# Performance work log

Hardware: AMD Instinct MI355X
Metric: run time of the kernel (lower is better)

Reference implementation:

```python
import jax, jax.numpy as jnp
import numpy as np

B = 8
N_GENES = 19836
D_IN = 11
D_H = 64
DEG = 16
N = B * N_GENES
E_PER = N_GENES * DEG


def setup_inputs() -> dict:
    key = jax.random.key(0)
    ks = jax.random.split(key, 20)
    x = jax.random.normal(ks[0], (B, N_GENES, D_IN), dtype=jnp.float32)
    # edges: random within each graph, offset by graph index
    base_src = jax.random.randint(ks[1], (B, E_PER), 0, N_GENES)
    base_dst = jax.random.randint(ks[2], (B, E_PER), 0, N_GENES)
    offs = (jnp.arange(B) * N_GENES)[:, None]
    src = (base_src + offs).reshape(-1).astype(jnp.int64) if False else (base_src + offs).reshape(-1)
    dst = (base_dst + offs).reshape(-1)
    s = 0.02
    def nrm(k, shape):
        return jax.random.normal(k, shape, dtype=jnp.float32) * s
    return {
        'x': x, 'src': src, 'dst': dst,
        'enc_W': nrm(ks[3], (D_H, D_IN)), 'enc_b': jnp.zeros((D_H,), jnp.float32),
        'gene_emb': nrm(ks[4], (N_GENES, D_H)),
        'gin_W': nrm(ks[5], (D_H, D_H)),
        'bn_w': 1.0 + nrm(ks[6], (D_H,)), 'bn_b': jnp.zeros((D_H,), jnp.float32),
        'key_W': nrm(ks[7], (D_H, D_H)), 'key_b': jnp.zeros((D_H,), jnp.float32),
        'query_w': nrm(ks[8], (1, D_H)),
        'val_W': nrm(ks[9], (D_H, D_H)), 'val_b': jnp.zeros((D_H,), jnp.float32),
        'sae_enc_W': nrm(ks[10], (D_H, D_H)), 'sae_enc_b': jnp.zeros((D_H,), jnp.float32),
        'sae_dec_W': nrm(ks[11], (D_H, D_H)), 'sae_dec_b': jnp.zeros((D_H,), jnp.float32),
        'pred_W1': nrm(ks[12], (D_H, D_H)), 'pred_b1': jnp.zeros((D_H,), jnp.float32),
        'pred_W2': nrm(ks[13], (1, D_H)), 'pred_b2': jnp.zeros((1,), jnp.float32),
    }


def gelu(x):
    return jax.nn.gelu(x, approximate=False)  # nn.GELU default = exact erf


def batchnorm(h, w, b, eps=1e-5):
    # training-mode BatchNorm1d: batch statistics, biased variance
    mu = jnp.mean(h, axis=0)
    var = jnp.mean((h - mu) ** 2, axis=0)
    return (h - mu) * jax.lax.rsqrt(var + eps) * w + b


def reference(x, src, dst, enc_W, enc_b, gene_emb, gin_W, bn_w, bn_b,
              key_W, key_b, query_w, val_W, val_b,
              sae_enc_W, sae_enc_b, sae_dec_W, sae_dec_b,
              pred_W1, pred_b1, pred_W2, pred_b2):
    bsz, n_gene, d_in = x.shape
    n_nodes = bsz * n_gene
    # gene encoder: single Linear (bias) + GELU (inner batchnorm result is discarded in source)
    h = gelu(x.reshape(-1, d_in) @ enc_W.T + enc_b)          # [N, D_H]
    h = (h.reshape(bsz, n_gene, -1) + gene_emb).reshape(n_nodes, -1)
    # GIN layer (eps=0, sum aggregation): MLP(h + sum_{u->v} h_u); MLP = single Linear, no bias
    agg = jax.ops.segment_sum(h[src], dst, num_segments=n_nodes)  # irregular gather/scatter
    h = (h + agg) @ gin_W.T
    h = gelu(batchnorm(h, bn_w, bn_b))
    # attentive readout with SAE
    keys = h @ key_W.T + key_b
    w = jax.nn.sigmoid(keys @ query_w.T)                     # [N, 1]
    v = h @ val_W.T + val_b
    z = v * w
    enc = jax.nn.relu(z @ sae_enc_W.T + sae_enc_b)
    dec = enc @ sae_dec_W.T + sae_dec_b
    sae_loss = jnp.mean((dec - z) ** 2) + 1.0 * jnp.mean(jnp.abs(enc))
    gid = jnp.arange(n_nodes) // n_gene
    g_h = jax.ops.segment_sum(dec * w, gid, num_segments=bsz)  # [B, D_H]
    # predictor: Linear+GELU, Linear (inner batchnorm discarded in source)
    preds = gelu(g_h @ pred_W1.T + pred_b1) @ pred_W2.T + pred_b2
    return preds, w, sae_loss, dec
```

## Files before the change

### kernel.cpp

```cpp
#include <hip/hip_runtime.h>
#include <hip/hip_bf16.h>
#include <math.h>

#define NGENES 19836
#define BATCH 8
#define DIN 11
#define DH 64
#define NNODES (BATCH * NGENES)
#define E_PER (NGENES * 16)
#define NEDGES (NNODES * 16)
#define NDH (NNODES * DH)
#define NWAVE ((NNODES + 63) / 64)
#define NBLK_NODE ((NWAVE + 3) / 4)

#define SCAN_CHUNK 1024
#define NSBLK ((NNODES + SCAN_CHUNK - 1) / SCAN_CHUNK)

#define OUT_PREDS 0
#define OUT_W 8
#define OUT_SAE (8 + NNODES)
#define OUT_DEC (9 + NNODES)

__device__ __forceinline__ float gelu_f(float x) {
    return 0.5f * x * (1.0f + erff(x * 0.70710678118654752f));
}

__device__ __forceinline__ float bcast(float v, int lane) {
    return __int_as_float(__builtin_amdgcn_readlane(__float_as_int(v), lane));
}

__device__ __forceinline__ float wave_sum(float v) {
    #pragma unroll
    for (int o = 32; o; o >>= 1) v += __shfl_xor(v, o, 64);
    return v;
}

__global__ void k_encoder(const float* __restrict__ x, const float* __restrict__ encW,
                          const float* __restrict__ encB, const float* __restrict__ gemb,
                          __hip_bfloat16* __restrict__ h16) {
    int lane = threadIdx.x & 63;
    int g = blockIdx.x & 7;
    int wix = (blockIdx.x >> 3) * (blockDim.x >> 6) + (threadIdx.x >> 6);
    int wper = (gridDim.x >> 3) * (blockDim.x >> 6);
    float wreg[DIN];
    #pragma unroll
    for (int k = 0; k < DIN; ++k) wreg[k] = encW[lane * DIN + k];
    float bias = encB[lane];
    size_t gb = (size_t)g * NGENES;
    for (int i = wix; i < NGENES; i += wper) {
        size_t node = gb + i;
        const float* xr = x + node * DIN;
        float acc = bias;
        #pragma unroll
        for (int k = 0; k < DIN; ++k) acc = fmaf(xr[k], wreg[k], acc);
        float hv = gelu_f(acc) + gemb[(size_t)i * DH + lane];
        h16[node * DH + lane] = __float2bfloat16(hv);
    }
}

__global__ void k_hist(const int* __restrict__ dst, int* __restrict__ counts) {
    int g = blockIdx.x & 7;
    int t = (blockIdx.x >> 3) * blockDim.x + threadIdx.x;
    int nt = (gridDim.x >> 3) * blockDim.x;
    const int* dg = dst + (size_t)g * E_PER;
    for (int e = t; e < E_PER; e += nt)
        atomicAdd(&counts[dg[e]], 1);
}

__global__ void k_scan1(const int* __restrict__ counts, int* __restrict__ bsum) {
    __shared__ int red[256];
    int base = blockIdx.x * SCAN_CHUNK + threadIdx.x * 4;
    int s = 0;
    #pragma unroll
    for (int i = 0; i < 4; ++i) {
        int n = base + i;
        if (n < NNODES) s += counts[n];
    }
    red[threadIdx.x] = s;
    __syncthreads();
    for (int o = 128; o; o >>= 1) {
        if (threadIdx.x < o) red[threadIdx.x] += red[threadIdx.x + o];
        __syncthreads();
    }
    if (threadIdx.x == 0) bsum[blockIdx.x] = red[0];
}

__global__ void k_scan2(const int* __restrict__ bsum, int* __restrict__ boff) {
    __shared__ int red[256];
    int t = threadIdx.x;
    int v = (t < NSBLK) ? bsum[t] : 0;
    red[t] = v;
    __syncthreads();
    for (int o = 1; o < 256; o <<= 1) {
        int u = (t >= o) ? red[t - o] : 0;
        __syncthreads();
        red[t] += u;
        __syncthreads();
    }
    if (t < NSBLK) boff[t] = red[t] - v;
}

__global__ void k_scan3(const int* __restrict__ counts, const int* __restrict__ boff,
                        int* __restrict__ offsets, int* __restrict__ cursor) {
    __shared__ int red[256];
    int t = threadIdx.x;
    int base = blockIdx.x * SCAN_CHUNK + t * 4;
    int c[4];
    int s = 0;
    #pragma unroll
    for (int i = 0; i < 4; ++i) {
        int n = base + i;
        c[i] = (n < NNODES) ? counts[n] : 0;
        s += c[i];
    }
    red[t] = s;
    __syncthreads();
    for (int o = 1; o < 256; o <<= 1) {
        int v = (t >= o) ? red[t - o] : 0;
        __syncthreads();
        red[t] += v;
        __syncthreads();
    }
    int excl = red[t] - s + boff[blockIdx.x];
    #pragma unroll
    for (int i = 0; i < 4; ++i) {
        int n = base + i;
        if (n < NNODES) { offsets[n] = excl; cursor[n] = excl; }
        excl += c[i];
    }
}

__global__ void k_scatter(const int* __restrict__ src, const int* __restrict__ dst,
                          int* __restrict__ cursor, unsigned short* __restrict__ csr) {
    int g = blockIdx.x & 7;
    int t = (blockIdx.x >> 3) * blockDim.x + threadIdx.x;
    int nt = (gridDim.x >> 3) * blockDim.x;
    const int* sg = src + (size_t)g * E_PER;
    const int* dg = dst + (size_t)g * E_PER;
    int gbase = g * NGENES;
    for (int e = t; e < E_PER; e += nt) {
        int p = atomicAdd(&cursor[dg[e]], 1);
        csr[p] = (unsigned short)(sg[e] - gbase);
    }
}

__global__ void __launch_bounds__(256, 4)
k_aggin(const __hip_bfloat16* __restrict__ h16, const int* __restrict__ offsets,
        const int* __restrict__ counts, const unsigned short* __restrict__ csr,
        const float* __restrict__ ginW, float* __restrict__ h2,
        float* __restrict__ stats) {
    __shared__ float ldsW[DH * DH];
    __shared__ float red[2][256];
    for (int idx = threadIdx.x; idx < DH * DH; idx += 256) {
        int k = idx >> 6, d = idx & 63;
        ldsW[idx] = ginW[d * DH + k];
    }
    __syncthreads();
    int lane = threadIdx.x & 63;
    int g = blockIdx.x & 7;
    int wix = (blockIdx.x >> 3) * 4 + (threadIdx.x >> 6);
    int wper = (gridDim.x >> 3) * 4;
    int gbase = g * NGENES;
    float s1 = 0.f, s2 = 0.f;
    for (int i = wix; i < NGENES; i += wper) {
        int node = gbase + i;
        float a[8];
        a[0] = __bfloat162float(h16[(size_t)node * DH + lane]);
        #pragma unroll
        for (int u = 1; u < 8; ++u) a[u] = 0.f;
        int start = offsets[node];
        int cnt = counts[node];
        for (int e0 = 0; e0 < cnt; e0 += 64) {
            int nn = min(64, cnt - e0);
            int iv = (lane < nn) ? (int)csr[start + e0 + lane] : 0;
            int j = 0;
            for (; j + 7 < nn; j += 8) {
                #pragma unroll
                for (int u = 0; u < 8; ++u) {
                    int v = gbase + __shfl(iv, j + u, 64);
                    a[u] += __bfloat162float(h16[(size_t)v * DH + lane]);
                }
            }
            for (; j < nn; ++j)
                a[0] += __bfloat162float(h16[(size_t)(gbase + __shfl(iv, j, 64)) * DH + lane]);
        }
        float tval = ((a[0] + a[1]) + (a[2] + a[3])) + ((a[4] + a[5]) + (a[6] + a[7]));
        float m0 = 0.f, m1 = 0.f, m2 = 0.f, m3 = 0.f;
        #pragma unroll
        for (int k = 0; k < DH; k += 4) {
            m0 = fmaf(ldsW[(k + 0) * DH + lane], bcast(tval, k + 0), m0);
            m1 = fmaf(ldsW[(k + 1) * DH + lane], bcast(tval, k + 1), m1);
            m2 = fmaf(ldsW[(k + 2) * DH + lane], bcast(tval, k + 2), m2);
            m3 = fmaf(ldsW[(k + 3) * DH + lane], bcast(tval, k + 3), m3);
        }
        float outv = (m0 + m1) + (m2 + m3);
        h2[(size_t)node * DH + lane] = outv;
        s1 += outv;
        s2 += outv * outv;
    }
    red[0][threadIdx.x] = s1;
    red[1][threadIdx.x] = s2;
    __syncthreads();
    if (threadIdx.x < 64) {
        float t1 = red[0][threadIdx.x] + red[0][threadIdx.x + 64] + red[0][threadIdx.x + 128] + red[0][threadIdx.x + 192];
        float t2 = red[1][threadIdx.x] + red[1][threadIdx.x + 64] + red[1][threadIdx.x + 128] + red[1][threadIdx.x + 192];
        atomicAdd(&stats[threadIdx.x], t1);
        atomicAdd(&stats[64 + threadIdx.x], t2);
    }
}

__global__ void k_bnparams(const float* __restrict__ stats, const float* __restrict__ bnw,
                           const float* __restrict__ bnb, const float* __restrict__ keyW,
                           const float* __restrict__ keyB, const float* __restrict__ qw,
                           float* __restrict__ bnp) {
    int d = threadIdx.x;
    float inv_n = 1.0f / (float)NNODES;
    float mu = stats[d] * inv_n;
    float var = stats[64 + d] * inv_n - mu * mu;
    float sc = bnw[d] * rsqrtf(var + 1e-5f);
    bnp[d] = sc;
    bnp[64 + d] = bnb[d] - mu * sc;
    float kq0 = 0.f, kq1 = 0.f;
    #pragma unroll
    for (int j = 0; j < DH; j += 2) {
        kq0 = fmaf(qw[j], keyW[j * DH + d], kq0);
        kq1 = fmaf(qw[j + 1], keyW[(j + 1) * DH + d], kq1);
    }
    bnp[128 + d] = kq0 + kq1;
    float qb = wave_sum(qw[d] * keyB[d]);
    if (d == 0) bnp[192] = qb;
}

__global__ void __launch_bounds__(256, 2)
k_attn(float* __restrict__ h2, const float* __restrict__ bnp,
       const float* __restrict__ valW, const float* __restrict__ valB,
       float* __restrict__ wout) {
    int lane = threadIdx.x & 63;
    int wv = (blockIdx.x * blockDim.x + threadIdx.x) >> 6;
    int node = wv * 64 + lane;
    if (node >= NNODES) return;
    float* row = h2 + (size_t)node * DH;
    float h3[DH];
    #pragma unroll
    for (int j = 0; j < 16; ++j) {
        float4 v = *reinterpret_cast<const float4*>(row + j * 4);
        h3[j * 4] = v.x; h3[j * 4 + 1] = v.y; h3[j * 4 + 2] = v.z; h3[j * 4 + 3] = v.w;
    }
    float p = bnp[192];
    #pragma unroll
    for (int k = 0; k < DH; ++k) {
        h3[k] = gelu_f(fmaf(h3[k], bnp[k], bnp[64 + k]));
        p = fmaf(h3[k], bnp[128 + k], p);
    }
    float wq = 1.0f / (1.0f + expf(-p));
    wout[node] = wq;
    #pragma unroll 1
    for (int d4 = 0; d4 < DH; d4 += 4) {
        float a0 = valB[d4], a1 = valB[d4 + 1], a2 = valB[d4 + 2], a3 = valB[d4 + 3];
        #pragma unroll
        for (int k = 0; k < DH; ++k) {
            a0 = fmaf(valW[(d4 + 0) * DH + k], h3[k], a0);
            a1 = fmaf(valW[(d4 + 1) * DH + k], h3[k], a1);
            a2 = fmaf(valW[(d4 + 2) * DH + k], h3[k], a2);
            a3 = fmaf(valW[(d4 + 3) * DH + k], h3[k], a3);
        }
        float4 v = { a0 * wq, a1 * wq, a2 * wq, a3 * wq };
        *reinterpret_cast<float4*>(row + d4) = v;
    }
}

__global__ void __launch_bounds__(256, 2)
k_saenc(const float* __restrict__ zbuf, const float* __restrict__ encW,
        const float* __restrict__ encB, float* __restrict__ encout,
        float* __restrict__ loss) {
    int lane = threadIdx.x & 63;
    int wv = (blockIdx.x * blockDim.x + threadIdx.x) >> 6;
    int node = wv * 64 + lane;
    bool act = node < NNODES;
    const float* zr = zbuf + (size_t)node * DH;
    float z[DH];
    if (act) {
        #pragma unroll
        for (int j = 0; j < 16; ++j) {
            float4 v = *reinterpret_cast<const float4*>(zr + j * 4);
            z[j * 4] = v.x; z[j * 4 + 1] = v.y; z[j * 4 + 2] = v.z; z[j * 4 + 3] = v.w;
        }
    } else {
        #pragma unroll
        for (int k = 0; k < DH; ++k) z[k] = 0.f;
    }
    float l1 = 0.f;
    float* er = encout + (size_t)node * DH;
    #pragma unroll 1
    for (int d4 = 0; d4 < DH; d4 += 4) {
        float a0 = encB[d4], a1 = encB[d4 + 1], a2 = encB[d4 + 2], a3 = encB[d4 + 3];
        #pragma unroll
        for (int k = 0; k < DH; ++k) {
            a0 = fmaf(encW[(d4 + 0) * DH + k], z[k], a0);
            a1 = fmaf(encW[(d4 + 1) * DH + k], z[k], a1);
            a2 = fmaf(encW[(d4 + 2) * DH + k], z[k], a2);
            a3 = fmaf(encW[(d4 + 3) * DH + k], z[k], a3);
        }
        a0 = fmaxf(a0, 0.f); a1 = fmaxf(a1, 0.f);
        a2 = fmaxf(a2, 0.f); a3 = fmaxf(a3, 0.f);
        l1 += (a0 + a1) + (a2 + a3);
        if (act) {
            float4 v = { a0, a1, a2, a3 };
            *reinterpret_cast<float4*>(er + d4) = v;
        }
    }
    if (!act) l1 = 0.f;
    l1 = wave_sum(l1);
    if (lane == 0) atomicAdd(&loss[1], l1);
}

__global__ void __launch_bounds__(256, 2)
k_saedec(const float* __restrict__ zbuf, const float* __restrict__ decW,
         const float* __restrict__ decB, float* __restrict__ decout,
         float* __restrict__ loss) {
    int lane = threadIdx.x & 63;
    int wv = (blockIdx.x * blockDim.x + threadIdx.x) >> 6;
    int node = wv * 64 + lane;
    bool act = node < NNODES;
    float* dr = decout + (size_t)node * DH;
    const float* zr = zbuf + (size_t)node * DH;
    float enc[DH];
    if (act) {
        #pragma unroll
        for (int j = 0; j < 16; ++j) {
            float4 v = *reinterpret_cast<const float4*>(dr + j * 4);
            enc[j * 4] = v.x; enc[j * 4 + 1] = v.y; enc[j * 4 + 2] = v.z; enc[j * 4 + 3] = v.w;
        }
    } else {
        #pragma unroll
        for (int k = 0; k < DH; ++k) enc[k] = 0.f;
    }
    float sq = 0.f;
    #pragma unroll 1
    for (int d4 = 0; d4 < DH; d4 += 4) {
        float a0 = decB[d4], a1 = decB[d4 + 1], a2 = decB[d4 + 2], a3 = decB[d4 + 3];
        #pragma unroll
        for (int k = 0; k < DH; ++k) {
            a0 = fmaf(decW[(d4 + 0) * DH + k], enc[k], a0);
            a1 = fmaf(decW[(d4 + 1) * DH + k], enc[k], a1);
            a2 = fmaf(decW[(d4 + 2) * DH + k], enc[k], a2);
            a3 = fmaf(decW[(d4 + 3) * DH + k], enc[k], a3);
        }
        if (act) {
            float4 zv = *reinterpret_cast<const float4*>(zr + d4);
            float d0 = a0 - zv.x, d1 = a1 - zv.y, d2 = a2 - zv.z, d3 = a3 - zv.w;
            sq += (d0 * d0 + d1 * d1) + (d2 * d2 + d3 * d3);
            float4 v = { a0, a1, a2, a3 };
            *reinterpret_cast<float4*>(dr + d4) = v;
        }
    }
    sq = wave_sum(sq);
    if (lane == 0) atomicAdd(&loss[0], sq);
}

__global__ void k_ghsum(const float* __restrict__ dec, const float* __restrict__ wout,
                        float* __restrict__ g_h) {
    int lane = threadIdx.x & 63;
    int wid = (blockIdx.x * blockDim.x + threadIdx.x) >> 6;
    int tw = (gridDim.x * blockDim.x) >> 6;
    int chunk = (NNODES + tw - 1) / tw;
    int gs = wid * chunk;
    int ge = min(gs + chunk, NNODES);
    if (gs >= ge) return;
    float gacc = 0.f;
    int cur_g = gs / NGENES;
    for (int n = gs; n < ge; ++n) {
        int g = n / NGENES;
        if (g != cur_g) {
            atomicAdd(&g_h[cur_g * DH + lane], gacc);
            gacc = 0.f;
            cur_g = g;
        }
        gacc = fmaf(dec[(size_t)n * DH + lane], wout[n], gacc);
    }
    atomicAdd(&g_h[cur_g * DH + lane], gacc);
}

__global__ void k_pred(const float* __restrict__ g_h, const float* __restrict__ W1,
                       const float* __restrict__ b1, const float* __restrict__ W2,
                       const float* __restrict__ b2, const float* __restrict__ loss,
                       float* __restrict__ out) {
    int lane = threadIdx.x;
    float w1[DH];
    #pragma unroll
    for (int k = 0; k < DH; ++k) w1[k] = W1[lane * DH + k];
    float bb = b1[lane], w2 = W2[lane];
    for (int g = 0; g < BATCH; ++g) {
        float gh = g_h[g * DH + lane];
        float a0 = 0.f, a1 = 0.f;
        #pragma unroll
        for (int k = 0; k < DH; k += 2) {
            a0 = fmaf(w1[k], bcast(gh, k), a0);
            a1 = fmaf(w1[k + 1], bcast(gh, k + 1), a1);
        }
        float t = gelu_f(a0 + a1 + bb);
        float p = wave_sum(t * w2);
        if (lane == 0) out[OUT_PREDS + g] = p + b2[0];
    }
    if (lane == 0) out[OUT_SAE] = (loss[0] + loss[1]) * (1.0f / ((float)NNODES * (float)DH));
}

extern "C" void kernel_launch(void* const* d_in, const int* in_sizes, int n_in,
                              void* d_out, int out_size, void* d_ws, size_t ws_size,
                              hipStream_t stream) {
    const float* x    = (const float*)d_in[0];
    const int* src    = (const int*)d_in[1];
    const int* dst    = (const int*)d_in[2];
    const float* encW = (const float*)d_in[3];
    const float* encB = (const float*)d_in[4];
    const float* gemb = (const float*)d_in[5];
    const float* ginW = (const float*)d_in[6];
    const float* bnw  = (const float*)d_in[7];
    const float* bnb  = (const float*)d_in[8];
    const float* keyW = (const float*)d_in[9];
    const float* keyB = (const float*)d_in[10];
    const float* qw   = (const float*)d_in[11];
    const float* valW = (const float*)d_in[12];
    const float* valB = (const float*)d_in[13];
    const float* saeEncW = (const float*)d_in[14];
    const float* saeEncB = (const float*)d_in[15];
    const float* saeDecW = (const float*)d_in[16];
    const float* saeDecB = (const float*)d_in[17];
    const float* pW1  = (const float*)d_in[18];
    const float* pb1  = (const float*)d_in[19];
    const float* pW2  = (const float*)d_in[20];
    const float* pb2  = (const float*)d_in[21];

    float* out = (float*)d_out;
    float* ws = (float*)d_ws;

    int*   counts  = (int*)ws;
    float* stats   = ws + NNODES;
    float* g_h     = stats + 128;
    float* loss    = g_h + 512;
    float* bnp     = loss + 2;
    int*   offsets = (int*)(bnp + 256);
    int*   cursor  = offsets + NNODES;
    unsigned short* csr = (unsigned short*)(cursor + NNODES);
    int*   bsum    = (int*)(csr + NEDGES);
    int*   boff    = bsum + 256;
    float* h2      = (float*)(boff + 256);

    __hip_bfloat16* h16 = (__hip_bfloat16*)(out + OUT_DEC);
    float* decregion = out + OUT_DEC;
    float* wout = out + OUT_W;

    hipMemsetAsync(d_ws, 0, (size_t)(NNODES + 642) * sizeof(float), stream);

    k_encoder<<<2048, 256, 0, stream>>>(x, encW, encB, gemb, h16);
    k_hist<<<2048, 256, 0, stream>>>(dst, counts);
    k_scan1<<<NSBLK, 256, 0, stream>>>(counts, bsum);
    k_scan2<<<1, 256, 0, stream>>>(bsum, boff);
    k_scan3<<<NSBLK, 256, 0, stream>>>(counts, boff, offsets, cursor);
    k_scatter<<<2048, 256, 0, stream>>>(src, dst, cursor, csr);
    k_aggin<<<2048, 256, 0, stream>>>(h16, offsets, counts, csr, ginW, h2, stats);
    k_bnparams<<<1, 64, 0, stream>>>(stats, bnw, bnb, keyW, keyB, qw, bnp);
    k_attn<<<NBLK_NODE, 256, 0, stream>>>(h2, bnp, valW, valB, wout);
    k_saenc<<<NBLK_NODE, 256, 0, stream>>>(h2, saeEncW, saeEncB, decregion, loss);
    k_saedec<<<NBLK_NODE, 256, 0, stream>>>(h2, saeDecW, saeDecB, decregion, loss);
    k_ghsum<<<512, 256, 0, stream>>>(decregion, wout, g_h);
    k_pred<<<1, 64, 0, stream>>>(g_h, pW1, pb1, pW2, pb2, loss, out);
}
```

Baseline: 812.3 us.

## Split aggregation from GIN matmul and store intermediates feature-major in bf16

The fused aggregate+GIN kernel is split into a gather-only kernel that writes bf16 sums and a per-node-thread matmul kernel. The matmul kernel writes its output feature-major (transposed) so that downstream per-thread kernels get coalesced loads. The z and encoder intermediates are stored in bf16, transposed, which halves their traffic and keeps the row-per-thread accesses coalesced. This adds one more kernel launch and introduces bf16 rounding of z/enc into the loss and dec computation, which risks accuracy.

```diff
diff --git a/kernel.cpp b/kernel.cpp
--- a/kernel.cpp
+++ b/kernel.cpp
@@ -10,8 +10,7 @@
 #define E_PER (NGENES * 16)
 #define NEDGES (NNODES * 16)
 #define NDH (NNODES * DH)
-#define NWAVE ((NNODES + 63) / 64)
-#define NBLK_NODE ((NWAVE + 3) / 4)
+#define NBLK_NODE ((NNODES + 255) / 256)
 
 #define SCAN_CHUNK 1024
 #define NSBLK ((NNODES + SCAN_CHUNK - 1) / SCAN_CHUNK)
@@ -145,23 +144,14 @@
 }
 
 __global__ void __launch_bounds__(256, 4)
-k_aggin(const __hip_bfloat16* __restrict__ h16, const int* __restrict__ offsets,
-        const int* __restrict__ counts, const unsigned short* __restrict__ csr,
-        const float* __restrict__ ginW, float* __restrict__ h2,
-        float* __restrict__ stats) {
-    __shared__ float ldsW[DH * DH];
-    __shared__ float red[2][256];
-    for (int idx = threadIdx.x; idx < DH * DH; idx += 256) {
-        int k = idx >> 6, d = idx & 63;
-        ldsW[idx] = ginW[d * DH + k];
-    }
-    __syncthreads();
+k_agg(const __hip_bfloat16* __restrict__ h16, const int* __restrict__ offsets,
+      const int* __restrict__ counts, const unsigned short* __restrict__ csr,
+      __hip_bfloat16* __restrict__ t) {
     int lane = threadIdx.x & 63;
     int g = blockIdx.x & 7;
     int wix = (blockIdx.x >> 3) * 4 + (threadIdx.x >> 6);
     int wper = (gridDim.x >> 3) * 4;
     int gbase = g * NGENES;
-    float s1 = 0.f, s2 = 0.f;
     for (int i = wix; i < NGENES; i += wper) {
         int node = gbase + i;
         float a[8];
@@ -185,27 +175,66 @@
                 a[0] += __bfloat162float(h16[(size_t)(gbase + __shfl(iv, j, 64)) * DH + lane]);
         }
         float tval = ((a[0] + a[1]) + (a[2] + a[3])) + ((a[4] + a[5]) + (a[6] + a[7]));
-        float m0 = 0.f, m1 = 0.f, m2 = 0.f, m3 = 0.f;
-        #pragma unroll
-        for (int k = 0; k < DH; k += 4) {
-            m0 = fmaf(ldsW[(k + 0) * DH + lane], bcast(tval, k + 0), m0);
-            m1 = fmaf(ldsW[(k + 1) * DH + lane], bcast(tval, k + 1), m1);
-            m2 = fmaf(ldsW[(k + 2) * DH + lane], bcast(tval, k + 2), m2);
-            m3 = fmaf(ldsW[(k + 3) * DH + lane], bcast(tval, k + 3), m3);
-        }
-        float outv = (m0 + m1) + (m2 + m3);
-        h2[(size_t)node * DH + lane] = outv;
-        s1 += outv;
-        s2 += outv * outv;
-    }
-    red[0][threadIdx.x] = s1;
-    red[1][threadIdx.x] = s2;
+        t[(size_t)node * DH + lane] = __float2bfloat16(tval);
+    }
+}
+
+__global__ void __launch_bounds__(256, 4)
+k_gin(const __hip_bfloat16* __restrict__ t, const float* __restrict__ ginW,
+      float* __restrict__ h2t, float* __restrict__ stats) {
+    __shared__ float ws[4][2][DH];
+    int lane = threadIdx.x & 63;
+    int w = threadIdx.x >> 6;
+    int node = blockIdx.x * 256 + threadIdx.x;
+    bool act = node < NNODES;
+    int nc = act ? node : 0;
+    const __hip_bfloat16* rp = t + (size_t)nc * DH;
+    float tr[DH];
+    #pragma unroll
+    for (int j = 0; j < 8; ++j) {
+        uint4 v = *reinterpret_cast<const uint4*>(rp + j * 8);
+        tr[j * 8 + 0] = __int_as_float(v.x << 16);
+        tr[j * 8 + 1] = __int_as_float(v.x & 0xffff0000u);
+        tr[j * 8 + 2] = __int_as_float(v.y << 16);
+        tr[j * 8 + 3] = __int_as_float(v.y & 0xffff0000u);
+        tr[j * 8 + 4] = __int_as_float(v.z << 16);
+        tr[j * 8 + 5] = __int_as_float(v.z & 0xffff0000u);
+        tr[j * 8 + 6] = __int_as_float(v.w << 16);
+        tr[j * 8 + 7] = __int_as_float(v.w & 0xffff0000u);
+    }
+    #pragma unroll 1
+    for (int d4 = 0; d4 < DH; d4 += 4) {
+        float s0 = 0.f, s1 = 0.f, s2 = 0.f, s3 = 0.f;
+        #pragma unroll
+        for (int k = 0; k < DH; ++k) {
+            float tk = tr[k];
+            s0 = fmaf(ginW[(d4 + 0) * DH + k], tk, s0);
+            s1 = fmaf(ginW[(d4 + 1) * DH + k], tk, s1);
+            s2 = fmaf(ginW[(d4 + 2) * DH + k], tk, s2);
+            s3 = fmaf(ginW[(d4 + 3) * DH + k], tk, s3);
+        }
+        if (act) {
+            h2t[(size_t)(d4 + 0) * NNODES + node] = s0;
+            h2t[(size_t)(d4 + 1) * NNODES + node] = s1;
+            h2t[(size_t)(d4 + 2) * NNODES + node] = s2;
+            h2t[(size_t)(d4 + 3) * NNODES + node] = s3;
+        } else { s0 = s1 = s2 = s3 = 0.f; }
+        float t0 = wave_sum(s0), t1 = wave_sum(s1);
+        float t2 = wave_sum(s2), t3 = wave_sum(s3);
+        float q0 = wave_sum(s0 * s0), q1 = wave_sum(s1 * s1);
+        float q2 = wave_sum(s2 * s2), q3 = wave_sum(s3 * s3);
+        if (lane == 0) {
+            ws[w][0][d4 + 0] = t0; ws[w][0][d4 + 1] = t1;
+            ws[w][0][d4 + 2] = t2; ws[w][0][d4 + 3] = t3;
+            ws[w][1][d4 + 0] = q0; ws[w][1][d4 + 1] = q1;
+            ws[w][1][d4 + 2] = q2; ws[w][1][d4 + 3] = q3;
+        }
+    }
     __syncthreads();
-    if (threadIdx.x < 64) {
-        float t1 = red[0][threadIdx.x] + red[0][threadIdx.x + 64] + red[0][threadIdx.x + 128] + red[0][threadIdx.x + 192];
-        float t2 = red[1][threadIdx.x] + red[1][threadIdx.x + 64] + red[1][threadIdx.x + 128] + red[1][threadIdx.x + 192];
-        atomicAdd(&stats[threadIdx.x], t1);
-        atomicAdd(&stats[64 + threadIdx.x], t2);
+    if (threadIdx.x < 128) {
+        int which = threadIdx.x >> 6, d = threadIdx.x & 63;
+        float s = ws[0][which][d] + ws[1][which][d] + ws[2][which][d] + ws[3][which][d];
+        atomicAdd(&stats[which * 64 + d], s);
     }
 }
 
@@ -231,82 +260,76 @@
     if (d == 0) bnp[192] = qb;
 }
 
-__global__ void __launch_bounds__(256, 2)
-k_attn(float* __restrict__ h2, const float* __restrict__ bnp,
-       const float* __restrict__ valW, const float* __restrict__ valB,
-       float* __restrict__ wout) {
-    int lane = threadIdx.x & 63;
-    int wv = (blockIdx.x * blockDim.x + threadIdx.x) >> 6;
-    int node = wv * 64 + lane;
-    if (node >= NNODES) return;
-    float* row = h2 + (size_t)node * DH;
+__global__ void __launch_bounds__(256, 4)
+k_postA(const float* __restrict__ h2t, const float* __restrict__ bnp,
+        const float* __restrict__ valW, const float* __restrict__ valB,
+        __hip_bfloat16* __restrict__ zt, float* __restrict__ wout) {
+    int node = blockIdx.x * 256 + threadIdx.x;
+    bool act = node < NNODES;
+    int nc = act ? node : 0;
     float h3[DH];
-    #pragma unroll
-    for (int j = 0; j < 16; ++j) {
-        float4 v = *reinterpret_cast<const float4*>(row + j * 4);
-        h3[j * 4] = v.x; h3[j * 4 + 1] = v.y; h3[j * 4 + 2] = v.z; h3[j * 4 + 3] = v.w;
-    }
     float p = bnp[192];
     #pragma unroll
     for (int k = 0; k < DH; ++k) {
-        h3[k] = gelu_f(fmaf(h3[k], bnp[k], bnp[64 + k]));
-        p = fmaf(h3[k], bnp[128 + k], p);
+        float hv = h2t[(size_t)k * NNODES + nc];
+        hv = gelu_f(fmaf(hv, bnp[k], bnp[64 + k]));
+        h3[k] = hv;
+        p = fmaf(hv, bnp[128 + k], p);
     }
     float wq = 1.0f / (1.0f + expf(-p));
-    wout[node] = wq;
+    if (act) wout[node] = wq;
     #pragma unroll 1
     for (int d4 = 0; d4 < DH; d4 += 4) {
-        float a0 = valB[d4], a1 = valB[d4 + 1], a2 = valB[d4 + 2], a3 = valB[d4 + 3];
+        float s0 = valB[d4 + 0], s1 = valB[d4 + 1], s2 = valB[d4 + 2], s3 = valB[d4 + 3];
         #pragma unroll
         for (int k = 0; k < DH; ++k) {
-            a0 = fmaf(valW[(d4 + 0) * DH + k], h3[k], a0);
-            a1 = fmaf(valW[(d4 + 1) * DH + k], h3[k], a1);
-            a2 = fmaf(valW[(d4 + 2) * DH + k], h3[k], a2);
-            a3 = fmaf(valW[(d4 + 3) * DH + k], h3[k], a3);
-        }
-        float4 v = { a0 * wq, a1 * wq, a2 * wq, a3 * wq };
-        *reinterpret_cast<float4*>(row + d4) = v;
-    }
-}
-
-__global__ void __launch_bounds__(256, 2)
-k_saenc(const float* __restrict__ zbuf, const float* __restrict__ encW,
-        const float* __restrict__ encB, float* __restrict__ encout,
+            float hk = h3[k];
+            s0 = fmaf(valW[(d4 + 0) * DH + k], hk, s0);
+            s1 = fmaf(valW[(d4 + 1) * DH + k], hk, s1);
+            s2 = fmaf(valW[(d4 + 2) * DH + k], hk, s2);
+            s3 = fmaf(valW[(d4 + 3) * DH + k], hk, s3);
+        }
+        if (act) {
+            zt[(size_t)(d4 + 0) * NNODES + node] = __float2bfloat16(s0 * wq);
+            zt[(size_t)(d4 + 1) * NNODES + node] = __float2bfloat16(s1 * wq);
+            zt[(size_t)(d4 + 2) * NNODES + node] = __float2bfloat16(s2 * wq);
+            zt[(size_t)(d4 + 3) * NNODES + node] = __float2bfloat16(s3 * wq);
+        }
+    }
+}
+
+__global__ void __launch_bounds__(256, 4)
+k_postB(const __hip_bfloat16* __restrict__ zt, const float* __restrict__ encW,
+        const float* __restrict__ encB, __hip_bfloat16* __restrict__ enct,
         float* __restrict__ loss) {
     int lane = threadIdx.x & 63;
-    int wv = (blockIdx.x * blockDim.x + threadIdx.x) >> 6;
-    int node = wv * 64 + lane;
+    int node = blockIdx.x * 256 + threadIdx.x;
     bool act = node < NNODES;
-    const float* zr = zbuf + (size_t)node * DH;
-    float z[DH];
-    if (act) {
-        #pragma unroll
-        for (int j = 0; j < 16; ++j) {
-            float4 v = *reinterpret_cast<const float4*>(zr + j * 4);
-            z[j * 4] = v.x; z[j * 4 + 1] = v.y; z[j * 4 + 2] = v.z; z[j * 4 + 3] = v.w;
-        }
-    } else {
-        #pragma unroll
-        for (int k = 0; k < DH; ++k) z[k] = 0.f;
-    }
+    int nc = act ? node : 0;
+    float z64[DH];
+    #pragma unroll
+    for (int k = 0; k < DH; ++k)
+        z64[k] = __bfloat162float(zt[(size_t)k * NNODES + nc]);
     float l1 = 0.f;
-    float* er = encout + (size_t)node * DH;
     #pragma unroll 1
     for (int d4 = 0; d4 < DH; d4 += 4) {
-        float a0 = encB[d4], a1 = encB[d4 + 1], a2 = encB[d4 + 2], a3 = encB[d4 + 3];
+        float s0 = encB[d4 + 0], s1 = encB[d4 + 1], s2 = encB[d4 + 2], s3 = encB[d4 + 3];
         #pragma unroll
         for (int k = 0; k < DH; ++k) {
-            a0 = fmaf(encW[(d4 + 0) * DH + k], z[k], a0);
-            a1 = fmaf(encW[(d4 + 1) * DH + k], z[k], a1);
-            a2 = fmaf(encW[(d4 + 2) * DH + k], z[k], a2);
-            a3 = fmaf(encW[(d4 + 3) * DH + k], z[k], a3);
-        }
-        a0 = fmaxf(a0, 0.f); a1 = fmaxf(a1, 0.f);
-        a2 = fmaxf(a2, 0.f); a3 = fmaxf(a3, 0.f);
-        l1 += (a0 + a1) + (a2 + a3);
+            float zk = z64[k];
+            s0 = fmaf(encW[(d4 + 0) * DH + k], zk, s0);
+            s1 = fmaf(encW[(d4 + 1) * DH + k], zk, s1);
+            s2 = fmaf(encW[(d4 + 2) * DH + k], zk, s2);
+            s3 = fmaf(encW[(d4 + 3) * DH + k], zk, s3);
+        }
+        s0 = fmaxf(s0, 0.f); s1 = fmaxf(s1, 0.f);
+        s2 = fmaxf(s2, 0.f); s3 = fmaxf(s3, 0.f);
+        l1 += (s0 + s1) + (s2 + s3);
         if (act) {
-            float4 v = { a0, a1, a2, a3 };
-            *reinterpret_cast<float4*>(er + d4) = v;
+            enct[(size_t)(d4 + 0) * NNODES + node] = __float2bfloat16(s0);
+            enct[(size_t)(d4 + 1) * NNODES + node] = __float2bfloat16(s1);
+            enct[(size_t)(d4 + 2) * NNODES + node] = __float2bfloat16(s2);
+            enct[(size_t)(d4 + 3) * NNODES + node] = __float2bfloat16(s3);
         }
     }
     if (!act) l1 = 0.f;
@@ -314,46 +337,43 @@
     if (lane == 0) atomicAdd(&loss[1], l1);
 }
 
-__global__ void __launch_bounds__(256, 2)
-k_saedec(const float* __restrict__ zbuf, const float* __restrict__ decW,
-         const float* __restrict__ decB, float* __restrict__ decout,
-         float* __restrict__ loss) {
-    int lane = threadIdx.x & 63;
-    int wv = (blockIdx.x * blockDim.x + threadIdx.x) >> 6;
-    int node = wv * 64 + lane;
+__global__ void __launch_bounds__(256, 4)
+k_postC(const __hip_bfloat16* __restrict__ enct, const __hip_bfloat16* __restrict__ zt,
+        const float* __restrict__ decW, const float* __restrict__ decB,
+        float* __restrict__ decout, float* __restrict__ loss) {
+    int lane = threadIdx.x & 63;
+    int node = blockIdx.x * 256 + threadIdx.x;
     bool act = node < NNODES;
-    float* dr = decout + (size_t)node * DH;
-    const float* zr = zbuf + (size_t)node * DH;
-    float enc[DH];
-    if (act) {
-        #pragma unroll
-        for (int j = 0; j < 16; ++j) {
-            float4 v = *reinterpret_cast<const float4*>(dr + j * 4);
-            enc[j * 4] = v.x; enc[j * 4 + 1] = v.y; enc[j * 4 + 2] = v.z; enc[j * 4 + 3] = v.w;
-        }
-    } else {
-        #pragma unroll
-        for (int k = 0; k < DH; ++k) enc[k] = 0.f;
-    }
+    int nc = act ? node : 0;
+    float e64[DH];
+    #pragma unroll
+    for (int k = 0; k < DH; ++k)
+        e64[k] = __bfloat162float(enct[(size_t)k * NNODES + nc]);
     float sq = 0.f;
+    float* dr = decout + (size_t)nc * DH;
     #pragma unroll 1
     for (int d4 = 0; d4 < DH; d4 += 4) {
-        float a0 = decB[d4], a1 = decB[d4 + 1], a2 = decB[d4 + 2], a3 = decB[d4 + 3];
+        float s0 = decB[d4 + 0], s1 = decB[d4 + 1], s2 = decB[d4 + 2], s3 = decB[d4 + 3];
         #pragma unroll
         for (int k = 0; k < DH; ++k) {
-            a0 = fmaf(decW[(d4 + 0) * DH + k], enc[k], a0);
-            a1 = fmaf(decW[(d4 + 1) * DH + k], enc[k], a1);
-            a2 = fmaf(decW[(d4 + 2) * DH + k], enc[k], a2);
-            a3 = fmaf(decW[(d4 + 3) * DH + k], enc[k], a3);
-        }
+            float ek = e64[k];
+            s0 = fmaf(decW[(d4 + 0) * DH + k], ek, s0);
+            s1 = fmaf(decW[(d4 + 1) * DH + k], ek, s1);
+            s2 = fmaf(decW[(d4 + 2) * DH + k], ek, s2);
+            s3 = fmaf(decW[(d4 + 3) * DH + k], ek, s3);
+        }
+        float z0 = __bfloat162float(zt[(size_t)(d4 + 0) * NNODES + nc]);
+        float z1 = __bfloat162float(zt[(size_t)(d4 + 1) * NNODES + nc]);
+        float z2 = __bfloat162float(zt[(size_t)(d4 + 2) * NNODES + nc]);
+        float z3 = __bfloat162float(zt[(size_t)(d4 + 3) * NNODES + nc]);
+        float d0 = s0 - z0, d1 = s1 - z1, d2 = s2 - z2, d3 = s3 - z3;
+        sq += (d0 * d0 + d1 * d1) + (d2 * d2 + d3 * d3);
         if (act) {
-            float4 zv = *reinterpret_cast<const float4*>(zr + d4);
-            float d0 = a0 - zv.x, d1 = a1 - zv.y, d2 = a2 - zv.z, d3 = a3 - zv.w;
-            sq += (d0 * d0 + d1 * d1) + (d2 * d2 + d3 * d3);
-            float4 v = { a0, a1, a2, a3 };
+            float4 v = { s0, s1, s2, s3 };
             *reinterpret_cast<float4*>(dr + d4) = v;
         }
     }
+    if (!act) sq = 0.f;
     sq = wave_sum(sq);
     if (lane == 0) atomicAdd(&loss[0], sq);
 }
@@ -438,19 +458,23 @@
     float* stats   = ws + NNODES;
     float* g_h     = stats + 128;
     float* loss    = g_h + 512;
-    float* bnp     = loss + 2;
+    float* bnp     = loss + 4;
     int*   offsets = (int*)(bnp + 256);
     int*   cursor  = offsets + NNODES;
     unsigned short* csr = (unsigned short*)(cursor + NNODES);
     int*   bsum    = (int*)(csr + NEDGES);
     int*   boff    = bsum + 256;
-    float* h2      = (float*)(boff + 256);
+    float* h2t     = (float*)(boff + 256);
+    __hip_bfloat16* t = (__hip_bfloat16*)(h2t + NDH);
+
+    __hip_bfloat16* zt   = t;
+    __hip_bfloat16* enct = (__hip_bfloat16*)h2t;
 
     __hip_bfloat16* h16 = (__hip_bfloat16*)(out + OUT_DEC);
     float* decregion = out + OUT_DEC;
     float* wout = out + OUT_W;
 
-    hipMemsetAsync(d_ws, 0, (size_t)(NNODES + 642) * sizeof(float), stream);
+    hipMemsetAsync(d_ws, 0, (size_t)(NNODES + 648) * sizeof(float), stream);
 
     k_encoder<<<2048, 256, 0, stream>>>(x, encW, encB, gemb, h16);
     k_hist<<<2048, 256, 0, stream>>>(dst, counts);
@@ -458,11 +482,12 @@
     k_scan2<<<1, 256, 0, stream>>>(bsum, boff);
     k_scan3<<<NSBLK, 256, 0, stream>>>(counts, boff, offsets, cursor);
     k_scatter<<<2048, 256, 0, stream>>>(src, dst, cursor, csr);
-    k_aggin<<<2048, 256, 0, stream>>>(h16, offsets, counts, csr, ginW, h2, stats);
+    k_agg<<<2048, 256, 0, stream>>>(h16, offsets, counts, csr, t);
+    k_gin<<<NBLK_NODE, 256, 0, stream>>>(t, ginW, h2t, stats);
     k_bnparams<<<1, 64, 0, stream>>>(stats, bnw, bnb, keyW, keyB, qw, bnp);
-    k_attn<<<NBLK_NODE, 256, 0, stream>>>(h2, bnp, valW, valB, wout);
-    k_saenc<<<NBLK_NODE, 256, 0, stream>>>(h2, saeEncW, saeEncB, decregion, loss);
-    k_saedec<<<NBLK_NODE, 256, 0, stream>>>(h2, saeDecW, saeDecB, decregion, loss);
+    k_postA<<<NBLK_NODE, 256, 0, stream>>>(h2t, bnp, valW, valB, zt, wout);
+    k_postB<<<NBLK_NODE, 256, 0, stream>>>(zt, saeEncW, saeEncB, enct, loss);
+    k_postC<<<NBLK_NODE, 256, 0, stream>>>(enct, zt, saeDecW, saeDecB, decregion, loss);
     k_ghsum<<<512, 256, 0, stream>>>(decregion, wout, g_h);
     k_pred<<<1, 64, 0, stream>>>(g_h, pW1, pb1, pW2, pb2, loss, out);
 }
```

Measured after the change: 1.023 ms. +25.9%, slower.
